# Kernel optimization log

Measured on AMD Instinct MI355X. Metric: run time of the kernel, lower is better.

Reference implementation:

```python
import jax, jax.numpy as jnp
import numpy as np
from jax import lax

KERNELS = (3, 5, 7, 9, 11, 13, 15)
H = W = 4096


def _box_mean(x, k):
    """2D box-mean filter with replicate (edge) padding, computed separably.

    Edge padding is separable, so (pad2d -> kxk box) == (padH -> kx1 box -> padW -> 1xk box).
    x: [N, 1, H, W]
    """
    p = k // 2
    kh = jnp.full((1, 1, k, 1), 1.0 / k, dtype=x.dtype)
    kw = jnp.full((1, 1, 1, k), 1.0 / k, dtype=x.dtype)
    dn = ('NCHW', 'OIHW', 'NCHW')
    y = jnp.pad(x, ((0, 0), (0, 0), (p, p), (0, 0)), mode='edge')
    y = lax.conv_general_dilated(y, kh, (1, 1), 'VALID', dimension_numbers=dn)
    y = jnp.pad(y, ((0, 0), (0, 0), (0, 0), (p, p)), mode='edge')
    y = lax.conv_general_dilated(y, kw, (1, 1), 'VALID', dimension_numbers=dn)
    return y


def setup_inputs() -> dict:
    key = jax.random.key(0)
    k1, k2 = jax.random.split(key)
    x = jax.random.uniform(k1, (1, 1, H, W), dtype=jnp.float32)
    # binary occupancy-style map, as float (torch uses mapU8 -> fp16 multiply)
    map_mask = (jax.random.uniform(k2, (H, W)) > 0.5).astype(jnp.float32)
    return {"x": x, "map_mask": map_mask}


def reference(x, map_mask):
    # sum of 7 multi-scale box means, averaged, then masked by the map
    acc = _box_mean(x, KERNELS[0])
    for k in KERNELS[1:]:
        acc = acc + _box_mean(x, k)
    out = acc / len(KERNELS)
    return out * map_mask[None, None, :, :]
```

## Files before the change

### kernel.cpp

```cpp
#include <hip/hip_runtime.h>


#define TILE   64
#define HALO   7
#define LHX    8
#define NCOL   80
#define NROW   78
#define PSTR   83
#define PROWSA 81
#define HH     4096
#define WW     4096

__global__ __launch_bounds__(256) void meanconv_kernel(
    const float* __restrict__ x, const float* __restrict__ mask,
    float* __restrict__ out)
{
    __shared__ float P[PROWSA * PSTR];
    const int tid = threadIdx.x;
    const int c0  = blockIdx.x * TILE;
    const int r0  = blockIdx.y * TILE;

    if (tid < 81) P[tid] = 0.0f;

    const bool xint = (c0 >= LHX) && (c0 - LHX + NCOL <= WW);

    for (int idx = tid; idx < NROW * 4; idx += 256) {
        const int lr  = idx >> 2;
        const int s   = idx & 3;
        const int gr  = min(max(r0 + lr - HALO, 0), HH - 1);
        const int gc0 = c0 - LHX + 20 * s;
        float v[20];
        if (xint) {
            const float* src = &x[(size_t)gr * WW + gc0];
            #pragma unroll
            for (int q = 0; q < 5; ++q) {
                const float4 t = *(const float4*)(src + 4 * q);
                v[4*q+0] = t.x; v[4*q+1] = t.y; v[4*q+2] = t.z; v[4*q+3] = t.w;
            }
        } else {
            #pragma unroll
            for (int i = 0; i < 20; ++i) {
                const int gc = min(max(gc0 + i, 0), WW - 1);
                v[i] = x[(size_t)gr * WW + gc];
            }
        }
        #pragma unroll
        for (int i = 1; i < 20; ++i) v[i] += v[i - 1];
        const float tot = v[19];
        float sum = tot;
        float u = __shfl_up(sum, 1, 4); if (s >= 1) sum += u;
        u       = __shfl_up(sum, 2, 4); if (s >= 2) sum += u;
        const float off = sum - tot;
        float* dst = &P[(lr + 1) * PSTR + 1 + 20 * s];
        #pragma unroll
        for (int i = 0; i < 20; ++i) dst[i] = v[i] + off;
    }
    __syncthreads();

    for (int idx = tid; idx < 80 * 4; idx += 256) {
        const int c  = (idx >> 2) + 1;
        const int s  = idx & 3;
        const int rs = 1 + 20 * s;
        float v[20];
        float run = 0.0f;
        #pragma unroll
        for (int i = 0; i < 20; ++i) {
            const int r = rs + i;
            float t = P[r * PSTR + c];
            t = (r < 79) ? t : 0.0f;
            run += t; v[i] = run;
        }
        const float tot = run;
        float sum = tot;
        float u = __shfl_up(sum, 1, 4); if (s >= 1) sum += u;
        u       = __shfl_up(sum, 2, 4); if (s >= 2) sum += u;
        const float off = sum - tot;
        #pragma unroll
        for (int i = 0; i < 20; ++i) {
            const int r = rs + i;
            if (r < 79) P[r * PSTR + c] = v[i] + off;
        }
    }
    __syncthreads();

    const int g  = tid & 7;
    const int ty = tid >> 3;
    const int B0 = 8 * g;
    #pragma unroll
    for (int j = 0; j < 2; ++j) {
        const int rr = ty + 32 * j;
        const int A  = rr + HALO;
        float a[8] = {0.f,0.f,0.f,0.f,0.f,0.f,0.f,0.f};
        #pragma unroll
        for (int p = 1; p <= 7; ++p) {
            const int   k = 2 * p + 1;
            const float w = 1.0f / (7.0f * (float)(k * k));
            const float* rT = &P[(A - p) * PSTR];
            const float* rB = &P[(A + p + 1) * PSTR];
            const int cl = B0 + LHX - p;
            const int cr = cl + 2 * p + 1;
            #pragma unroll
            for (int i = 0; i < 8; ++i) {
                a[i] += w * (rB[cr + i] - rT[cr + i] - rB[cl + i] + rT[cl + i]);
            }
        }
        const int gr = r0 + rr, gc = c0 + B0;
        const float4 m0 = *(const float4*)&mask[(size_t)gr * WW + gc];
        const float4 m1 = *(const float4*)&mask[(size_t)gr * WW + gc + 4];
        float4 o0, o1;
        o0.x = a[0] * m0.x; o0.y = a[1] * m0.y; o0.z = a[2] * m0.z; o0.w = a[3] * m0.w;
        o1.x = a[4] * m1.x; o1.y = a[5] * m1.y; o1.z = a[6] * m1.z; o1.w = a[7] * m1.w;
        *(float4*)&out[(size_t)gr * WW + gc]     = o0;
        *(float4*)&out[(size_t)gr * WW + gc + 4] = o1;
    }
}

extern "C" void kernel_launch(void* const* d_in, const int* in_sizes, int n_in,
                              void* d_out, int out_size, void* d_ws, size_t ws_size,
                              hipStream_t stream) {
    const float* x    = (const float*)d_in[0];
    const float* mask = (const float*)d_in[1];
    float*       out  = (float*)d_out;
    dim3 grid(WW / TILE, HH / TILE);
    meanconv_kernel<<<grid, 256, 0, stream>>>(x, mask, out);
}
```

Before: 184.0 us.

## Vectorize shared-memory prefix table access and swizzle tile order

Realigns the shared prefix-sum table to a 16-byte-aligned stride of 84 and drops the padding column, so row prefix sums are stored and the box-difference stage reads with float4 LDS operations instead of scalar ones. Linearizes the grid and remaps block IDs so consecutive blocks are spread across tile rows, likely to balance work across XCDs or improve L2 locality. Adds a launch_bounds occupancy hint of 6. The extra registers for the float4 windows in the final stage risk spilling or lower occupancy.

```diff
diff --git a/kernel.cpp b/kernel.cpp
--- a/kernel.cpp
+++ b/kernel.cpp
@@ -6,21 +6,24 @@
 #define LHX    8
 #define NCOL   80
 #define NROW   78
-#define PSTR   83
-#define PROWSA 81
+#define PSTR   84
+#define PROWS  79
 #define HH     4096
 #define WW     4096
 
-__global__ __launch_bounds__(256) void meanconv_kernel(
+__global__ __launch_bounds__(256, 6) void meanconv_kernel(
     const float* __restrict__ x, const float* __restrict__ mask,
     float* __restrict__ out)
 {
-    __shared__ float P[PROWSA * PSTR];
+    __shared__ __align__(16) float P[PROWS * PSTR];
     const int tid = threadIdx.x;
-    const int c0  = blockIdx.x * TILE;
-    const int r0  = blockIdx.y * TILE;
 
-    if (tid < 81) P[tid] = 0.0f;
+    const int lid  = blockIdx.x;
+    const int tile = ((lid & 7) << 9) | (lid >> 3);
+    const int c0   = (tile & 63) * TILE;
+    const int r0   = (tile >> 6) * TILE;
+
+    if (tid < PSTR) P[tid] = 0.0f;
 
     const bool xint = (c0 >= LHX) && (c0 - LHX + NCOL <= WW);
 
@@ -51,14 +54,19 @@
         float u = __shfl_up(sum, 1, 4); if (s >= 1) sum += u;
         u       = __shfl_up(sum, 2, 4); if (s >= 2) sum += u;
         const float off = sum - tot;
-        float* dst = &P[(lr + 1) * PSTR + 1 + 20 * s];
+        float* dst = &P[(lr + 1) * PSTR + 20 * s];
         #pragma unroll
-        for (int i = 0; i < 20; ++i) dst[i] = v[i] + off;
+        for (int q = 0; q < 5; ++q) {
+            float4 t;
+            t.x = v[4*q+0] + off; t.y = v[4*q+1] + off;
+            t.z = v[4*q+2] + off; t.w = v[4*q+3] + off;
+            *(float4*)(dst + 4 * q) = t;
+        }
     }
     __syncthreads();
 
     for (int idx = tid; idx < 80 * 4; idx += 256) {
-        const int c  = (idx >> 2) + 1;
+        const int c  = idx >> 2;
         const int s  = idx & 3;
         const int rs = 1 + 20 * s;
         float v[20];
@@ -66,8 +74,8 @@
         #pragma unroll
         for (int i = 0; i < 20; ++i) {
             const int r = rs + i;
-            float t = P[r * PSTR + c];
-            t = (r < 79) ? t : 0.0f;
+            float t = 0.0f;
+            if (r < PROWS) t = P[r * PSTR + c];
             run += t; v[i] = run;
         }
         const float tot = run;
@@ -78,7 +86,7 @@
         #pragma unroll
         for (int i = 0; i < 20; ++i) {
             const int r = rs + i;
-            if (r < 79) P[r * PSTR + c] = v[i] + off;
+            if (r < PROWS) P[r * PSTR + c] = v[i] + off;
         }
     }
     __syncthreads();
@@ -93,15 +101,25 @@
         float a[8] = {0.f,0.f,0.f,0.f,0.f,0.f,0.f,0.f};
         #pragma unroll
         for (int p = 1; p <= 7; ++p) {
-            const int   k = 2 * p + 1;
-            const float w = 1.0f / (7.0f * (float)(k * k));
-            const float* rT = &P[(A - p) * PSTR];
-            const float* rB = &P[(A + p + 1) * PSTR];
-            const int cl = B0 + LHX - p;
-            const int cr = cl + 2 * p + 1;
+            const int   k   = 2 * p + 1;
+            const float w   = 1.0f / (7.0f * (float)(k * k));
+            const int   al  = (7 - p) & ~3;
+            const int   lo  = (7 - p) - al;
+            const int   ro  = (8 + p) - al;
+            const int   nf4 = (15 + p - al) / 4 + 1;
+            const float4* rT4 = (const float4*)&P[(A - p)     * PSTR + B0 + al];
+            const float4* rB4 = (const float4*)&P[(A + p + 1) * PSTR + B0 + al];
+            float wT[24], wB[24];
+            #pragma unroll
+            for (int q = 0; q < nf4; ++q) {
+                const float4 t = rT4[q];
+                wT[4*q+0] = t.x; wT[4*q+1] = t.y; wT[4*q+2] = t.z; wT[4*q+3] = t.w;
+                const float4 b = rB4[q];
+                wB[4*q+0] = b.x; wB[4*q+1] = b.y; wB[4*q+2] = b.z; wB[4*q+3] = b.w;
+            }
             #pragma unroll
             for (int i = 0; i < 8; ++i) {
-                a[i] += w * (rB[cr + i] - rT[cr + i] - rB[cl + i] + rT[cl + i]);
+                a[i] += w * ((wB[ro + i] - wT[ro + i]) - (wB[lo + i] - wT[lo + i]));
             }
         }
         const int gr = r0 + rr, gc = c0 + B0;
@@ -121,6 +139,5 @@
     const float* x    = (const float*)d_in[0];
     const float* mask = (const float*)d_in[1];
     float*       out  = (float*)d_out;
-    dim3 grid(WW / TILE, HH / TILE);
-    meanconv_kernel<<<grid, 256, 0, stream>>>(x, mask, out);
+    meanconv_kernel<<<dim3(64 * 64), 256, 0, stream>>>(x, mask, out);
 }
```

Measured after the change: 204.5 us. +11.2%, slower.
